# Kernel optimization log

Hardware: AMD Instinct MI355X
Metric: run time of the kernel (lower is better)

## Reference

```python
import jax, jax.numpy as jnp
import numpy as np

def setup_inputs() -> dict:
    key = jax.random.key(0)
    x = jax.random.normal(key, (2, 16, 2048, 64), dtype=jnp.float32)
    return {"x": x}

def reference(x):
    # Unnormalized attention: scores = q k^T (no softmax, no scaling), out = scores v,
    # with q = k = v = x. Faithful to the two torch.einsum calls.
    scores = jnp.einsum('bhid,bhjd->bhij', x, x)   # [B,H,T,T]
    out = jnp.einsum('bhij,bhjd->bhid', scores, x)  # [B,H,T,D]
    return out
```

## Files before the change

### kernel.cpp

```cpp
#include <hip/hip_runtime.h>


#define TDIM 2048
#define DDIM 64
#define NHEADS 32
#define NCH 16

#define PART_FLOATS ((size_t)NHEADS * NCH * 4096)

typedef float f4 __attribute__((ext_vector_type(4)));
typedef float f32x4 __attribute__((ext_vector_type(4)));
typedef short bf16x8 __attribute__((ext_vector_type(8)));
typedef short s4 __attribute__((ext_vector_type(4)));

__device__ __forceinline__ void async_copy16(const void* g, void* l) {
    __builtin_amdgcn_global_load_lds(
        (const __attribute__((address_space(1))) void*)g,
        (__attribute__((address_space(3))) void*)l, 16, 0, 0);
}

__device__ __forceinline__ short f2bf(float f) {
    unsigned u = __builtin_bit_cast(unsigned, f);
    unsigned r = (u + 0x7fffu + ((u >> 16) & 1u)) >> 16;
    return (short)r;
}

__device__ __forceinline__ const bf16x8* fragp(const short* base, int row,
                                               int rowlen, int kelem) {
    const char* p = (const char*)(base + row * rowlen);
    return (const bf16x8*)(p + ((kelem * 2) ^ ((row & 7) << 4)));
}

__global__ __launch_bounds__(256) void k1_gram(const float* __restrict__ x,
                                               float* __restrict__ part) {
    __shared__ __align__(16) short XT[64 * 128];

    const int b    = blockIdx.x;
    const int tid  = threadIdx.x;
    const int lane = tid & 63;
    const int w    = tid >> 6;
    const int head = b >> 4, ch = b & 15;

    const float* xh = x + ((size_t)head * TDIM + ch * 128) * DDIM;

#pragma unroll
    for (int e = 0; e < 8; ++e) {
        const int i4 = e * 256 + tid;
        const int r  = i4 >> 4;
        const int c4 = (i4 & 15) << 2;
        const f4 v = *reinterpret_cast<const f4*>(xh + (size_t)i4 * 4);
#pragma unroll
        for (int j = 0; j < 4; ++j) {
            const int c = c4 + j;
            *(short*)((char*)XT + c * 256 + ((2 * r) ^ ((c & 7) << 4))) =
                f2bf(v[j]);
        }
    }
    __syncthreads();

    const int li = lane & 15, g = lane >> 4;
    const int iq0 = (w >> 1) * 2, jq0 = (w & 1) * 2;

    f32x4 acc[2][2];
#pragma unroll
    for (int a = 0; a < 2; ++a)
#pragma unroll
        for (int q = 0; q < 2; ++q) acc[a][q] = (f32x4){0.f, 0.f, 0.f, 0.f};

#pragma unroll
    for (int k0 = 0; k0 < 128; k0 += 32) {
        bf16x8 af[2], bv[2];
        af[0] = *fragp(XT, (iq0 + 0) * 16 + li, 128, k0 + 8 * g);
        af[1] = *fragp(XT, (iq0 + 1) * 16 + li, 128, k0 + 8 * g);
        bv[0] = *fragp(XT, (jq0 + 0) * 16 + li, 128, k0 + 8 * g);
        bv[1] = *fragp(XT, (jq0 + 1) * 16 + li, 128, k0 + 8 * g);
#pragma unroll
        for (int a = 0; a < 2; ++a)
#pragma unroll
            for (int q = 0; q < 2; ++q)
                acc[a][q] = __builtin_amdgcn_mfma_f32_16x16x32_bf16(
                    af[a], bv[q], acc[a][q], 0, 0, 0);
    }

    float* pp = part + (size_t)b * 4096;
#pragma unroll
    for (int a = 0; a < 2; ++a)
#pragma unroll
        for (int d = 0; d < 2; ++d)
#pragma unroll
            for (int q = 0; q < 4; ++q)
                pp[((iq0 + a) * 16 + g * 4 + q) * 64 + (jq0 + d) * 16 + li] =
                    acc[a][d][q];
}

__global__ __launch_bounds__(256) void k2a_reduce(const float* __restrict__ part,
                                                  short* __restrict__ gbf) {
    const int b    = blockIdx.x;
    const int tid  = threadIdx.x;
    const int head = b >> 2, p = b & 3;

    const int idx4 = p * 1024 + tid * 4;
    const float* ph = part + (size_t)head * NCH * 4096 + idx4;

    f4 s = (f4){0.f, 0.f, 0.f, 0.f};
#pragma unroll
    for (int c = 0; c < NCH; ++c)
        s += *reinterpret_cast<const f4*>(ph + (size_t)c * 4096);

    const int i  = idx4 >> 6;
    const int j4 = idx4 & 63;
    s4 pk;
    pk[0] = f2bf(s[0]); pk[1] = f2bf(s[1]);
    pk[2] = f2bf(s[2]); pk[3] = f2bf(s[3]);
    *(s4*)((char*)gbf + (size_t)head * 8192 + i * 128 +
           ((2 * j4) ^ ((i & 7) << 4))) = pk;
}

__global__ __launch_bounds__(256) void k2b_xg(const float* __restrict__ x,
                                              float* __restrict__ out,
                                              const short* __restrict__ gbf) {
    __shared__ __align__(16) float Sf[4096];
    __shared__ __align__(16) short Xb[4096];
    __shared__ __align__(16) short Gb[4096];

    const int b    = blockIdx.x;
    const int tid  = threadIdx.x;
    const int lane = tid & 63;
    const int w    = tid >> 6;
    const int head = b >> 5, ch = b & 31;

    const float* xh = x + ((size_t)head * TDIM + ch * 64) * DDIM;

    {
        const float* gs = xh + w * 1024 + lane * 4;
        float* ld = Sf + w * 1024;
        const short* gg = gbf + (size_t)head * 4096 + w * 1024 + lane * 8;
        short* lg = Gb + w * 1024;
#pragma unroll
        for (int it = 0; it < 4; ++it)
            async_copy16(gs + it * 256, ld + it * 256);
#pragma unroll
        for (int it = 0; it < 2; ++it)
            async_copy16(gg + it * 512, lg + it * 512);
    }
    __syncthreads();

#pragma unroll
    for (int e = 0; e < 4; ++e) {
        const int i4 = e * 256 + tid;
        const int r  = i4 >> 4;
        const int c4 = (i4 & 15) << 2;
        const f4 v = *reinterpret_cast<const f4*>(Sf + (size_t)i4 * 4);
        s4 pk;
        pk[0] = f2bf(v[0]); pk[1] = f2bf(v[1]);
        pk[2] = f2bf(v[2]); pk[3] = f2bf(v[3]);
        *(s4*)((char*)Xb + r * 128 + ((2 * c4) ^ ((r & 7) << 4))) = pk;
    }
    __syncthreads();

    const int li = lane & 15, g = lane >> 4;

    f32x4 acc[4];
#pragma unroll
    for (int d = 0; d < 4; ++d) acc[d] = (f32x4){0.f, 0.f, 0.f, 0.f};

#pragma unroll
    for (int k0 = 0; k0 < 64; k0 += 32) {
        bf16x8 af, bv[4];
        af = *fragp(Xb, w * 16 + li, 64, k0 + 8 * g);
#pragma unroll
        for (int d = 0; d < 4; ++d)
            bv[d] = *fragp(Gb, d * 16 + li, 64, k0 + 8 * g);
#pragma unroll
        for (int d = 0; d < 4; ++d)
            acc[d] = __builtin_amdgcn_mfma_f32_16x16x32_bf16(
                af, bv[d], acc[d], 0, 0, 0);
    }

    float* oh = out + ((size_t)head * TDIM + ch * 64) * DDIM;
#pragma unroll
    for (int d = 0; d < 4; ++d)
#pragma unroll
        for (int q = 0; q < 4; ++q)
            oh[(w * 16 + g * 4 + q) * 64 + d * 16 + li] = acc[d][q];
}

extern "C" void kernel_launch(void* const* d_in, const int* in_sizes, int n_in,
                              void* d_out, int out_size, void* d_ws, size_t ws_size,
                              hipStream_t stream) {
    const float* x = (const float*)d_in[0];
    float* out  = (float*)d_out;
    float* part = (float*)d_ws;
    short* gbf  = (short*)((float*)d_ws + PART_FLOATS);

    k1_gram<<<NHEADS * NCH, 256, 0, stream>>>(x, part);
    k2a_reduce<<<128, 256, 0, stream>>>(part, gbf);
    k2b_xg<<<NHEADS * 32, 256, 0, stream>>>(x, out, gbf);
}
```

Measured before the change: 20.42 us.

## Store Gram partials as bf16 in fragment order and streamline loads

Stores per-chunk Gram partials as bf16 in MFMA fragment order, which halves partial traffic and gives coalesced vector stores. The reduce kernel remaps indices back into the swizzled layout. The transpose into LDS now packs 8 rows per bf16x8 store instead of scalar short stores. The xg kernel loads x straight from global into registers instead of staging it through LDS. The cost is extra rounding, since the partials are truncated to bf16 before summation, which lowers accuracy.

```diff
diff --git a/kernel.cpp b/kernel.cpp
--- a/kernel.cpp
+++ b/kernel.cpp
@@ -6,8 +6,6 @@
 #define NHEADS 32
 #define NCH 16
 
-#define PART_FLOATS ((size_t)NHEADS * NCH * 4096)
-
 typedef float f4 __attribute__((ext_vector_type(4)));
 typedef float f32x4 __attribute__((ext_vector_type(4)));
 typedef short bf16x8 __attribute__((ext_vector_type(8)));
@@ -24,6 +22,9 @@
     unsigned r = (u + 0x7fffu + ((u >> 16) & 1u)) >> 16;
     return (short)r;
 }
+__device__ __forceinline__ float bf2f(short s) {
+    return __builtin_bit_cast(float, ((unsigned)(unsigned short)s) << 16);
+}
 
 __device__ __forceinline__ const bf16x8* fragp(const short* base, int row,
                                                int rowlen, int kelem) {
@@ -32,7 +33,7 @@
 }
 
 __global__ __launch_bounds__(256) void k1_gram(const float* __restrict__ x,
-                                               float* __restrict__ part) {
+                                               short* __restrict__ part) {
     __shared__ __align__(16) short XT[64 * 128];
 
     const int b    = blockIdx.x;
@@ -43,18 +44,21 @@
 
     const float* xh = x + ((size_t)head * TDIM + ch * 128) * DDIM;
 
-#pragma unroll
-    for (int e = 0; e < 8; ++e) {
-        const int i4 = e * 256 + tid;
-        const int r  = i4 >> 4;
-        const int c4 = (i4 & 15) << 2;
-        const f4 v = *reinterpret_cast<const f4*>(xh + (size_t)i4 * 4);
-#pragma unroll
-        for (int j = 0; j < 4; ++j) {
-            const int c = c4 + j;
-            *(short*)((char*)XT + c * 256 + ((2 * r) ^ ((c & 7) << 4))) =
-                f2bf(v[j]);
-        }
+    const int rg = tid >> 4, cg = tid & 15;
+    const int r0 = rg * 8, c4 = cg * 4;
+
+    f4 v[8];
+#pragma unroll
+    for (int k = 0; k < 8; ++k)
+        v[k] = *reinterpret_cast<const f4*>(xh + (size_t)(r0 + k) * DDIM + c4);
+
+#pragma unroll
+    for (int j = 0; j < 4; ++j) {
+        bf16x8 pk;
+#pragma unroll
+        for (int k = 0; k < 8; ++k) pk[k] = f2bf(v[k][j]);
+        const int c = c4 + j;
+        *(bf16x8*)((char*)XT + c * 256 + ((2 * r0) ^ ((c & 7) << 4))) = pk;
     }
     __syncthreads();
 
@@ -82,44 +86,51 @@
                     af[a], bv[q], acc[a][q], 0, 0, 0);
     }
 
-    float* pp = part + (size_t)b * 4096;
+    short* pp = part + (size_t)b * 4096;
 #pragma unroll
     for (int a = 0; a < 2; ++a)
 #pragma unroll
-        for (int d = 0; d < 2; ++d)
-#pragma unroll
-            for (int q = 0; q < 4; ++q)
-                pp[((iq0 + a) * 16 + g * 4 + q) * 64 + (jq0 + d) * 16 + li] =
-                    acc[a][d][q];
-}
-
-__global__ __launch_bounds__(256) void k2a_reduce(const float* __restrict__ part,
+        for (int d = 0; d < 2; ++d) {
+            s4 pk;
+#pragma unroll
+            for (int q = 0; q < 4; ++q) pk[q] = f2bf(acc[a][d][q]);
+            *(s4*)(pp + ((((w * 2 + a) * 2 + d) * 64 + lane) << 2)) = pk;
+        }
+}
+
+__global__ __launch_bounds__(256) void k2a_reduce(const short* __restrict__ part,
                                                   short* __restrict__ gbf) {
     const int b    = blockIdx.x;
     const int tid  = threadIdx.x;
-    const int head = b >> 2, p = b & 3;
-
-    const int idx4 = p * 1024 + tid * 4;
-    const float* ph = part + (size_t)head * NCH * 4096 + idx4;
-
-    f4 s = (f4){0.f, 0.f, 0.f, 0.f};
-#pragma unroll
-    for (int c = 0; c < NCH; ++c)
-        s += *reinterpret_cast<const f4*>(ph + (size_t)c * 4096);
-
-    const int i  = idx4 >> 6;
-    const int j4 = idx4 & 63;
-    s4 pk;
-    pk[0] = f2bf(s[0]); pk[1] = f2bf(s[1]);
-    pk[2] = f2bf(s[2]); pk[3] = f2bf(s[3]);
-    *(s4*)((char*)gbf + (size_t)head * 8192 + i * 128 +
-           ((2 * j4) ^ ((i & 7) << 4))) = pk;
+    const int head = b >> 2, quarter = b & 3;
+
+    const int f = quarter * 256 + tid;
+    const short* ph = part + (size_t)head * NCH * 4096 + (f << 2);
+
+    float s[4] = {0.f, 0.f, 0.f, 0.f};
+#pragma unroll
+    for (int c = 0; c < NCH; ++c) {
+        const s4 v = *reinterpret_cast<const s4*>(ph + (size_t)c * 4096);
+#pragma unroll
+        for (int q = 0; q < 4; ++q) s[q] += bf2f(v[q]);
+    }
+
+    const int lane = f & 63, wad = f >> 6;
+    const int w = wad >> 2, a = (wad >> 1) & 1, d = wad & 1;
+    const int g = lane >> 4, li = lane & 15;
+    const int iq0 = (w >> 1) * 2, jq0 = (w & 1) * 2;
+    const int j = (jq0 + d) * 16 + li;
+    char* gb = (char*)gbf + (size_t)head * 8192;
+#pragma unroll
+    for (int q = 0; q < 4; ++q) {
+        const int i = (iq0 + a) * 16 + g * 4 + q;
+        *(short*)(gb + i * 128 + ((2 * j) ^ ((i & 7) << 4))) = f2bf(s[q]);
+    }
 }
 
 __global__ __launch_bounds__(256) void k2b_xg(const float* __restrict__ x,
                                               float* __restrict__ out,
                                               const short* __restrict__ gbf) {
-    __shared__ __align__(16) float Sf[4096];
     __shared__ __align__(16) short Xb[4096];
     __shared__ __align__(16) short Gb[4096];
 
@@ -129,28 +140,21 @@
     const int w    = tid >> 6;
     const int head = b >> 5, ch = b & 31;
 
-    const float* xh = x + ((size_t)head * TDIM + ch * 64) * DDIM;
-
     {
-        const float* gs = xh + w * 1024 + lane * 4;
-        float* ld = Sf + w * 1024;
         const short* gg = gbf + (size_t)head * 4096 + w * 1024 + lane * 8;
         short* lg = Gb + w * 1024;
 #pragma unroll
-        for (int it = 0; it < 4; ++it)
-            async_copy16(gs + it * 256, ld + it * 256);
-#pragma unroll
         for (int it = 0; it < 2; ++it)
             async_copy16(gg + it * 512, lg + it * 512);
     }
-    __syncthreads();
-
+
+    const float* xh = x + ((size_t)head * TDIM + ch * 64) * DDIM;
 #pragma unroll
     for (int e = 0; e < 4; ++e) {
         const int i4 = e * 256 + tid;
         const int r  = i4 >> 4;
         const int c4 = (i4 & 15) << 2;
-        const f4 v = *reinterpret_cast<const f4*>(Sf + (size_t)i4 * 4);
+        const f4 v = *reinterpret_cast<const f4*>(xh + (size_t)i4 * 4);
         s4 pk;
         pk[0] = f2bf(v[0]); pk[1] = f2bf(v[1]);
         pk[2] = f2bf(v[2]); pk[3] = f2bf(v[3]);
@@ -190,8 +194,8 @@
                               hipStream_t stream) {
     const float* x = (const float*)d_in[0];
     float* out  = (float*)d_out;
-    float* part = (float*)d_ws;
-    short* gbf  = (short*)((float*)d_ws + PART_FLOATS);
+    short* part = (short*)d_ws;
+    short* gbf  = part + (size_t)512 * 4096;
 
     k1_gram<<<NHEADS * NCH, 256, 0, stream>>>(x, part);
     k2a_reduce<<<128, 256, 0, stream>>>(part, gbf);
```

Measured after the change: 18.98 us. 1.08x faster.
